# Performance work log

Measured on AMD Instinct MI355X. Metric: run time of the kernel, lower is better.

Reference implementation:

```python
import jax, jax.numpy as jnp
import numpy as np

H = 2        # attention heads (GENsConv heads=2)
DH = 128     # per-head dim (= hidden_channels; concat=False -> heads averaged)
L = 4        # num message-passing layers actually used (convs[:-1])
NG = 500     # number of graphs in the batch
N = 50000    # total nodes
E = 200000   # total edges
HID = 128    # hidden_channels
RES = 0.1    # initial_res
EPS = 1e-5   # BatchNorm eps (eval mode: running_mean=0, running_var=1)


def _bn(x, g, b):
    # BatchNorm1d in eval mode with default running stats
    return x * (g / jnp.sqrt(1.0 + EPS)) + b


def setup_inputs() -> dict:
    key = jax.random.key(0)
    ks = jax.random.split(key, 32)
    s = 0.05
    d = {}
    d["x"] = jax.random.randint(ks[0], (N,), 0, 30)
    d["edge_index"] = jax.random.randint(ks[1], (2, E), 0, N)
    d["edge_attr"] = jax.random.randint(ks[2], (E,), 0, 30)
    d["batch"] = jnp.sort(jax.random.randint(ks[3], (N,), 0, NG))
    d["node_emb"] = jax.random.normal(ks[4], (30, HID)) * s
    d["emb_w1"] = jax.random.normal(ks[5], (HID, HID)) * s
    d["emb_b1"] = jnp.zeros((HID,))
    d["emb_g1"] = jnp.ones((HID,))
    d["emb_bt1"] = jnp.zeros((HID,))
    d["emb_w2"] = jax.random.normal(ks[6], (HID, HID)) * s
    d["emb_b2"] = jnp.zeros((HID,))
    d["bn0_g"] = jnp.ones((HID,))
    d["bn0_b"] = jnp.zeros((HID,))
    d["Wq"] = jax.random.normal(ks[7], (L, HID, H * DH)) * s
    d["Wk"] = jax.random.normal(ks[8], (L, HID, H * DH)) * s
    d["Wv"] = jax.random.normal(ks[9], (L, HID, H * DH)) * s
    d["We"] = jax.random.normal(ks[10], (L, HID, H * DH)) * s
    d["att"] = jax.random.normal(ks[11], (L, H, DH)) * s
    d["Wroot"] = jax.random.normal(ks[12], (L, HID, HID)) * s
    d["bias"] = jnp.zeros((L, HID))
    d["out_w1"] = jax.random.normal(ks[13], (HID * (L + 1), HID)) * s
    d["out_b1"] = jnp.zeros((HID,))
    d["out_g1"] = jnp.ones((HID,))
    d["out_bt1"] = jnp.zeros((HID,))
    d["out_w2"] = jax.random.normal(ks[14], (HID, 1)) * s
    d["out_b2"] = jnp.zeros((1,))
    return d


def _forward(params, x, edge_index, edge_attr, batch):
    (node_emb, emb_w1, emb_b1, emb_g1, emb_bt1, emb_w2, emb_b2, bn0_g, bn0_b,
     Wq, Wk, Wv, We, att, Wroot, bias,
     out_w1, out_b1, out_g1, out_bt1, out_w2, out_b2) = params
    src, dst = edge_index[0], edge_index[1]
    h = node_emb[x]                      # [N, HID]
    ea = node_emb[edge_attr]             # [E, HID] (original embeds edge_attr with node_embedding)
    # emb_convs: Linear -> BN -> ReLU -> Linear, then bns[0] + ReLU
    h = jax.nn.relu(_bn(h @ emb_w1 + emb_b1, emb_g1, emb_bt1))
    h = h @ emb_w2 + emb_b2
    h = jax.nn.relu(_bn(h, bn0_g, bn0_b))
    x0 = h
    xs = [h]
    for i in range(L):
        hi = xs[-1]
        # gather -> per-edge multi-head attention message -> scatter (GENsConv stand-in)
        q = (hi @ Wq[i]).reshape(N, H, DH)[dst]          # [E, H, DH]
        k = (hi @ Wk[i]).reshape(N, H, DH)[src]
        v = (hi @ Wv[i]).reshape(N, H, DH)[src]
        e = (ea @ We[i]).reshape(E, H, DH)
        score = jnp.einsum('ehd,hd->eh', jax.nn.leaky_relu(q + k + e, 0.2), att[i])
        smax = jax.ops.segment_max(score, dst, num_segments=N)[dst]
        exps = jnp.exp(score - smax)
        denom = jax.ops.segment_sum(exps, dst, num_segments=N)[dst]
        alpha = exps / denom                              # segment softmax over incoming edges
        msg = alpha[..., None] * (v + e)                  # [E, H, DH]
        agg = jax.ops.segment_sum(msg, dst, num_segments=N)  # [N, H, DH]
        out = agg.mean(axis=1) + hi @ Wroot[i] + bias[i]  # concat=False -> average heads, + root
        out = jax.nn.relu(out)
        out = (1.0 - RES) * out + RES * x0                # initial residual
        xs.append(out)
    hc = jnp.concatenate(xs, axis=-1)                     # cat=True -> [N, HID*(L+1)]
    sums = jax.ops.segment_sum(hc, batch, num_segments=NG)
    cnt = jax.ops.segment_sum(jnp.ones((N, 1), hc.dtype), batch, num_segments=NG)
    g = sums / jnp.maximum(cnt, 1.0)                      # global mean pool
    g = jax.nn.relu(_bn(g @ out_w1 + out_b1, out_g1, out_bt1))
    g = g @ out_w2 + out_b2
    return g.reshape(-1)                                  # [NG]


def reference(x, edge_index, edge_attr, batch, node_emb, emb_w1, emb_b1, emb_g1, emb_bt1, emb_w2, emb_b2, bn0_g, bn0_b, Wq, Wk, Wv, We, att, Wroot, bias, out_w1, out_b1, out_g1, out_bt1, out_w2, out_b2):
    params = (node_emb, emb_w1, emb_b1, emb_g1, emb_bt1, emb_w2, emb_b2, bn0_g, bn0_b,
              Wq, Wk, Wv, We, att, Wroot, bias,
              out_w1, out_b1, out_g1, out_bt1, out_w2, out_b2)
    return _forward(params, x, edge_index, edge_attr, batch)
```

## Files before the change

### kernel.cpp

```cpp
#include <hip/hip_runtime.h>
#include <hip/hip_bf16.h>

#define NN 50000
#define NE 200000
#define NGR 500
#define HD 128
#define CDIM 256
#define NLAY 4
#define NVOC 30
#define NCAT 896
#define SCH 256
#define SNB ((NN + SCH - 1) / SCH)
#define GP 7
#define CBP (56 / GP)

#define SU_TBLN 30
#define SU_TBLE (NLAY * NVOC)
#define SU_PKW  (NLAY * 224 / 4)
#define SU_HIST ((NE + 255) / 256)
#define SU_NBLK (SU_TBLN + SU_TBLE + SU_PKW + SU_HIST)

static constexpr float BN_INV = 0.9999950000374997f;

typedef __attribute__((ext_vector_type(8))) short bf16x8;
typedef __attribute__((ext_vector_type(4))) float f32x4;
typedef __attribute__((ext_vector_type(2))) float f32x2;

__device__ __forceinline__ float bf2f(unsigned short u) {
    return __uint_as_float(((unsigned)u) << 16);
}
__device__ __forceinline__ unsigned short f2bf(float f) {
    union { __hip_bfloat16 h; unsigned short u; } cv;
    cv.h = __float2bfloat16(f);
    return cv.u;
}
__device__ __forceinline__ f32x2 up2(unsigned u) {
    f32x2 r;
    r.x = __uint_as_float(u << 16);
    r.y = __uint_as_float(u & 0xffff0000u);
    return r;
}
__device__ __forceinline__ f32x2 lk2(f32x2 z) {
    f32x2 zero = {0.f, 0.f};
    return __builtin_elementwise_max(z, zero) + 0.2f * __builtin_elementwise_min(z, zero);
}

__global__ __launch_bounds__(256) void k_setup(
    const float* __restrict__ ne,
    const float* __restrict__ w1, const float* __restrict__ b1,
    const float* __restrict__ g1, const float* __restrict__ bt1,
    const float* __restrict__ w2, const float* __restrict__ b2,
    const float* __restrict__ g0, const float* __restrict__ bt0,
    const float* __restrict__ We,
    const float* __restrict__ Wq, const float* __restrict__ Wk,
    const float* __restrict__ Wv, const float* __restrict__ Wr,
    const int* __restrict__ ei,
    float* __restrict__ x0tab, unsigned short* __restrict__ etab,
    unsigned short* __restrict__ Wpk, int* __restrict__ cnt)
{
    __shared__ float smem[256];
    int b = blockIdx.x, t = threadIdx.x;
    if (b < SU_TBLN) {
        int r = b, d = t;
        if (d < HD) smem[d] = ne[r * HD + d];
        __syncthreads();
        float v1 = 0.f;
        if (d < HD) {
            float acc = b1[d];
            for (int k = 0; k < HD; ++k) acc += smem[k] * w1[k * HD + d];
            v1 = fmaxf(acc * BN_INV * g1[d] + bt1[d], 0.f);
        }
        __syncthreads();
        if (d < HD) smem[HD + d] = v1;
        __syncthreads();
        if (d < HD) {
            float acc2 = b2[d];
            for (int k = 0; k < HD; ++k) acc2 += smem[HD + k] * w2[k * HD + d];
            x0tab[r * HD + d] = fmaxf(acc2 * BN_INV * g0[d] + bt0[d], 0.f);
        }
    } else if (b < SU_TBLN + SU_TBLE) {
        int la = b - SU_TBLN;
        int l = la / NVOC, a = la % NVOC;
        int c = t;
        if (c < HD) smem[c] = ne[a * HD + c];
        __syncthreads();
        const float* W = We + (size_t)l * HD * CDIM;
        float acc = 0.f;
        for (int k = 0; k < HD; ++k) acc += smem[k] * W[k * CDIM + c];
        etab[(size_t)la * CDIM + c] = f2bf(acc);
    } else if (b < SU_TBLN + SU_TBLE + SU_PKW) {
        int bb = (b - SU_TBLN - SU_TBLE) * 4 + (t >> 6);
        int lane = t & 63;
        int l = bb / 224, rem = bb % 224;
        int kb = rem / 56, jb = rem % 56;
        int j = jb * 16 + (lane & 15);
        int kbase = kb * 32 + ((lane >> 4) << 3);
        unsigned short* dst = Wpk + ((size_t)bb * 64 + lane) * 8;
#pragma unroll
        for (int tt = 0; tt < 8; ++tt) {
            int k = kbase + tt;
            float v;
            if (j < 256) {
                v = Wq[((size_t)l * HD + k) * CDIM + j];
            } else if (j < 768) {
                int t2 = j - 256, g = t2 >> 3, r = t2 & 7;
                int c = g * 4 + (r & 3);
                v = (r < 4) ? Wk[((size_t)l * HD + k) * CDIM + c]
                            : Wv[((size_t)l * HD + k) * CDIM + c];
            } else {
                v = Wr[((size_t)l * HD + k) * HD + (j - 768)];
            }
            dst[tt] = f2bf(v);
        }
    } else {
        int e = (b - SU_TBLN - SU_TBLE - SU_PKW) * 256 + t;
        if (e < NE) atomicAdd(&cnt[ei[NE + e]], 1);
    }
}

__global__ __launch_bounds__(256) void k_blocksum(const int* __restrict__ cnt, int* __restrict__ part)
{
    int t = threadIdx.x;
    int i = blockIdx.x * SCH + t;
    int v = (i < NN) ? cnt[i] : 0;
    __shared__ int sm[256];
    sm[t] = v;
    __syncthreads();
    for (int off = 128; off; off >>= 1) {
        if (t < off) sm[t] += sm[t + off];
        __syncthreads();
    }
    if (t == 0) part[blockIdx.x] = sm[0];
}

__global__ __launch_bounds__(256) void k_scanpart(int* __restrict__ part)
{
    int t = threadIdx.x;
    int v = (t < SNB) ? part[t] : 0;
    __shared__ int sm[256];
    sm[t] = v;
    __syncthreads();
    for (int off = 1; off < 256; off <<= 1) {
        int u = (t >= off) ? sm[t - off] : 0;
        __syncthreads();
        sm[t] += u;
        __syncthreads();
    }
    if (t < SNB) part[t] = sm[t] - v;
}

__global__ __launch_bounds__(256) void k_csrwrite(
    const int* __restrict__ cnt, const int* __restrict__ part,
    int* __restrict__ rowp, int* __restrict__ wof)
{
    int t = threadIdx.x;
    int i = blockIdx.x * SCH + t;
    int v = (i < NN) ? cnt[i] : 0;
    __shared__ int sm[256];
    sm[t] = v;
    __syncthreads();
    for (int off = 1; off < 256; off <<= 1) {
        int u = (t >= off) ? sm[t - off] : 0;
        __syncthreads();
        sm[t] += u;
        __syncthreads();
    }
    int excl = sm[t] - v + part[blockIdx.x];
    if (i < NN) { rowp[i] = excl; wof[i] = excl; }
    if (i == NN - 1) rowp[NN] = excl + v;
}

__global__ void k_scatter(const int* __restrict__ ei, const int* __restrict__ ea,
                          int* __restrict__ wof, int2* __restrict__ cse)
{
    int e = blockIdx.x * blockDim.x + threadIdx.x;
    if (e < NE) {
        int d = ei[NE + e];
        int pos = atomicAdd(&wof[d], 1);
        int2 v; v.x = ei[e]; v.y = ea[e];
        cse[pos] = v;
    }
}

__global__ void k_x0(const int* __restrict__ x, const float* __restrict__ tab,
                     unsigned short* __restrict__ x0b,
                     const int* __restrict__ batch, int* __restrict__ gptr)
{
    int idx = blockIdx.x * blockDim.x + threadIdx.x;
    if (idx <= NGR) {
        if (idx == NGR) gptr[idx] = NN;
        else {
            int lo = 0, hi = NN;
            while (lo < hi) { int mid = (lo + hi) >> 1; if (batch[mid] < idx) lo = mid + 1; else hi = mid; }
            gptr[idx] = lo;
        }
    }
    if (idx >= NN * 32) return;
    int n = idx >> 5, c = idx & 31;
    float4 v = *(const float4*)&tab[x[n] * HD + c * 4];
    ushort4 u; u.x = f2bf(v.x); u.y = f2bf(v.y); u.z = f2bf(v.z); u.w = f2bf(v.w);
    *(ushort4*)&x0b[(size_t)n * HD + c * 4] = u;
}

__global__ __launch_bounds__(256) void k_gemm(
    const unsigned short* __restrict__ Ab, const unsigned short* __restrict__ Wpk,
    unsigned short* __restrict__ C)
{
    __shared__ unsigned short tile[64][136];
    int lane = threadIdx.x & 63, wid = threadIdx.x >> 6;
    int nb = blockIdx.x * 64;
    int rowl = wid * 16 + (lane & 15);
    int node = nb + rowl;
    size_t arow = (size_t)((node < NN) ? node : (NN - 1));
    int ko = (lane >> 4) << 3;
    const unsigned short* ap = Ab + arow * HD + ko;
    bf16x8 a0 = *(const bf16x8*)(ap);
    bf16x8 a1 = *(const bf16x8*)(ap + 32);
    bf16x8 a2 = *(const bf16x8*)(ap + 64);
    bf16x8 a3 = *(const bf16x8*)(ap + 96);

    int cb0 = blockIdx.y * CBP;
    const unsigned short* bp = Wpk + (size_t)cb0 * 512 + (size_t)lane * 8;
    int jreg = (lane >> 4) << 2;
#pragma unroll 4
    for (int i = 0; i < CBP; ++i) {
        bf16x8 w0 = *(const bf16x8*)(bp + i * 512);
        bf16x8 w1 = *(const bf16x8*)(bp + i * 512 + 28672);
        bf16x8 w2 = *(const bf16x8*)(bp + i * 512 + 57344);
        bf16x8 w3 = *(const bf16x8*)(bp + i * 512 + 86016);
        f32x4 acc = {0.f, 0.f, 0.f, 0.f};
        acc = __builtin_amdgcn_mfma_f32_16x16x32_bf16(w0, a0, acc, 0, 0, 0);
        acc = __builtin_amdgcn_mfma_f32_16x16x32_bf16(w1, a1, acc, 0, 0, 0);
        acc = __builtin_amdgcn_mfma_f32_16x16x32_bf16(w2, a2, acc, 0, 0, 0);
        acc = __builtin_amdgcn_mfma_f32_16x16x32_bf16(w3, a3, acc, 0, 0, 0);
        uint2 o;
        o.x = (unsigned)f2bf(acc[0]) | ((unsigned)f2bf(acc[1]) << 16);
        o.y = (unsigned)f2bf(acc[2]) | ((unsigned)f2bf(acc[3]) << 16);
        *(uint2*)&tile[rowl][i * 16 + jreg] = o;
    }
    __syncthreads();
    int r0 = threadIdx.x >> 4;
    int cseg = (threadIdx.x & 15) * 8;
#pragma unroll
    for (int pass = 0; pass < 4; ++pass) {
        int row = pass * 16 + r0;
        int gnode = nb + row;
        if (gnode < NN) {
            uint4 v = *(const uint4*)&tile[row][cseg];
            *(uint4*)&C[(size_t)gnode * NCAT + cb0 * 16 + cseg] = v;
        }
    }
}

__global__ __launch_bounds__(256) void k_edge(
    const unsigned short* __restrict__ QKVR,
    const unsigned short* __restrict__ etab,
    const float* __restrict__ attL, const float* __restrict__ biasL,
    const unsigned short* __restrict__ x0b,
    const int* __restrict__ rowptr, const int2* __restrict__ cse,
    unsigned short* __restrict__ hb)
{
    int n = (blockIdx.x * blockDim.x + threadIdx.x) >> 6;
    if (n >= NN) return;
    int lane = threadIdx.x & 63;
    int head = lane >> 5, sub = lane & 31;
    int col = head * HD + sub * 4;
    int kvo = 256 + head * 256 + sub * 8;

    uint2 quu = *(const uint2*)&QKVR[(size_t)n * NCAT + col];
    f32x2 q0 = up2(quu.x), q1 = up2(quu.y);
    float4 a4 = *(const float4*)&attL[col];
    f32x2 av0 = {a4.x, a4.y}, av1 = {a4.z, a4.w};

    float l0 = 0.f, l1 = 0.f;
    f32x2 accA0 = {0.f, 0.f}, accA1 = {0.f, 0.f};
    f32x2 accB0 = {0.f, 0.f}, accB1 = {0.f, 0.f};

    int beg = rowptr[n], end = rowptr[n + 1];
    int idx = beg;
    for (; idx + 1 < end; idx += 2) {
        int2 seA = cse[idx];
        int2 seB = cse[idx + 1];
        uint4 kvA = *(const uint4*)&QKVR[(size_t)seA.x * NCAT + kvo];
        uint4 kvB = *(const uint4*)&QKVR[(size_t)seB.x * NCAT + kvo];
        uint2 euA = *(const uint2*)&etab[seA.y * CDIM + col];
        uint2 euB = *(const uint2*)&etab[seB.y * CDIM + col];

        f32x2 eA0 = up2(euA.x), eA1 = up2(euA.y);
        f32x2 eB0 = up2(euB.x), eB1 = up2(euB.y);

        f32x2 zA0 = lk2(q0 + up2(kvA.x) + eA0);
        f32x2 zA1 = lk2(q1 + up2(kvA.y) + eA1);
        f32x2 zB0 = lk2(q0 + up2(kvB.x) + eB0);
        f32x2 zB1 = lk2(q1 + up2(kvB.y) + eB1);

        f32x2 ppA = zA0 * av0 + zA1 * av1;
        f32x2 ppB = zB0 * av0 + zB1 * av1;
        float pA = ppA.x + ppA.y;
        float pB = ppB.x + ppB.y;
        pA += __shfl_xor(pA, 16); pB += __shfl_xor(pB, 16);
        pA += __shfl_xor(pA, 8);  pB += __shfl_xor(pB, 8);
        pA += __shfl_xor(pA, 4);  pB += __shfl_xor(pB, 4);
        pA += __shfl_xor(pA, 2);  pB += __shfl_xor(pB, 2);
        pA += __shfl_xor(pA, 1);  pB += __shfl_xor(pB, 1);
        float peA = __expf(fminf(fmaxf(pA, -30.f), 30.f));
        float peB = __expf(fminf(fmaxf(pB, -30.f), 30.f));

        accA0 += peA * (up2(kvA.z) + eA0);
        accA1 += peA * (up2(kvA.w) + eA1);
        accB0 += peB * (up2(kvB.z) + eB0);
        accB1 += peB * (up2(kvB.w) + eB1);
        l0 += peA;
        l1 += peB;
    }
    if (idx < end) {
        int2 se = cse[idx];
        uint4 kv = *(const uint4*)&QKVR[(size_t)se.x * NCAT + kvo];
        uint2 eu = *(const uint2*)&etab[se.y * CDIM + col];
        f32x2 e0 = up2(eu.x), e1 = up2(eu.y);
        f32x2 z0 = lk2(q0 + up2(kv.x) + e0);
        f32x2 z1 = lk2(q1 + up2(kv.y) + e1);
        f32x2 pp = z0 * av0 + z1 * av1;
        float p = pp.x + pp.y;
        p += __shfl_xor(p, 16); p += __shfl_xor(p, 8);
        p += __shfl_xor(p, 4);  p += __shfl_xor(p, 2); p += __shfl_xor(p, 1);
        float pe = __expf(fminf(fmaxf(p, -30.f), 30.f));
        accA0 += pe * (up2(kv.z) + e0);
        accA1 += pe * (up2(kv.w) + e1);
        l0 += pe;
    }
    float l = l0 + l1;
    float invl = (l > 0.f) ? 1.0f / l : 0.f;
    f32x2 r0 = (accA0 + accB0) * invl;
    f32x2 r1 = (accA1 + accB1) * invl;
    r0.x = 0.5f * (r0.x + __shfl_xor(r0.x, 32));
    r0.y = 0.5f * (r0.y + __shfl_xor(r0.y, 32));
    r1.x = 0.5f * (r1.x + __shfl_xor(r1.x, 32));
    r1.y = 0.5f * (r1.y + __shfl_xor(r1.y, 32));
    if (head == 0) {
        uint2 ruu = *(const uint2*)&QKVR[(size_t)n * NCAT + 768 + sub * 4];
        f32x2 ru0 = up2(ruu.x), ru1 = up2(ruu.y);
        float4 b4 = *(const float4*)&biasL[sub * 4];
        f32x2 bb0 = {b4.x, b4.y}, bb1 = {b4.z, b4.w};
        uint2 xuu = *(const uint2*)&x0b[(size_t)n * HD + sub * 4];
        f32x2 xx0 = up2(xuu.x), xx1 = up2(xuu.y);
        f32x2 zero = {0.f, 0.f};
        f32x2 h0 = 0.9f * __builtin_elementwise_max(r0 + ru0 + bb0, zero) + 0.1f * xx0;
        f32x2 h1 = 0.9f * __builtin_elementwise_max(r1 + ru1 + bb1, zero) + 0.1f * xx1;
        ushort4 o;
        o.x = f2bf(h0.x); o.y = f2bf(h0.y); o.z = f2bf(h1.x); o.w = f2bf(h1.y);
        *(ushort4*)&hb[(size_t)n * HD + sub * 4] = o;
    }
}

__global__ __launch_bounds__(256) void k_poolall(
    const unsigned short* __restrict__ x0b,
    const unsigned short* __restrict__ h0, const unsigned short* __restrict__ h1,
    const unsigned short* __restrict__ h2, const unsigned short* __restrict__ h3,
    const int* __restrict__ gptr, float* __restrict__ gsum)
{
    int g = blockIdx.x, sl = blockIdx.y;
    const unsigned short* src = (sl == 0) ? x0b : (sl == 1) ? h0 : (sl == 2) ? h1
                              : (sl == 3) ? h2 : h3;
    int q = threadIdx.x & 31;
    int r = threadIdx.x >> 5;
    int beg = gptr[g], end = gptr[g + 1];
    float sx = 0.f, sy = 0.f, sz = 0.f, sw = 0.f;
    for (int n = beg + r; n < end; n += 8) {
        uint2 u = *(const uint2*)&src[(size_t)n * HD + q * 4];
        sx += __uint_as_float(u.x << 16);
        sy += __uint_as_float(u.x & 0xffff0000u);
        sz += __uint_as_float(u.y << 16);
        sw += __uint_as_float(u.y & 0xffff0000u);
    }
    __shared__ float4 sm[8][32];
    float4 s4 = {sx, sy, sz, sw};
    sm[r][q] = s4;
    __syncthreads();
    if (r == 0) {
        float4 t = sm[0][q];
#pragma unroll
        for (int j = 1; j < 8; ++j) {
            float4 u = sm[j][q];
            t.x += u.x; t.y += u.y; t.z += u.z; t.w += u.w;
        }
        *(float4*)&gsum[(size_t)g * 640 + sl * HD + q * 4] = t;
    }
}

__global__ __launch_bounds__(128) void k_out(
    const float* __restrict__ gsum, const int* __restrict__ gptr,
    const float* __restrict__ w1, const float* __restrict__ b1,
    const float* __restrict__ g1, const float* __restrict__ bt1,
    const float* __restrict__ w2, const float* __restrict__ b2,
    float* __restrict__ out)
{
    int g = blockIdx.x, d = threadIdx.x;
    __shared__ float row[640];
    __shared__ float red[2];
    int c = gptr[g + 1] - gptr[g];
    float invc = 1.0f / (float)max(c, 1);
    for (int j = d; j < 640; j += 128) row[j] = gsum[(size_t)g * 640 + j] * invc;
    __syncthreads();
    float acc = b1[d];
    for (int j = 0; j < 640; ++j) acc += row[j] * w1[j * HD + d];
    float val = fmaxf(acc * BN_INV * g1[d] + bt1[d], 0.f);
    float part = val * w2[d];
    part += __shfl_xor(part, 32); part += __shfl_xor(part, 16);
    part += __shfl_xor(part, 8);  part += __shfl_xor(part, 4);
    part += __shfl_xor(part, 2);  part += __shfl_xor(part, 1);
    if ((threadIdx.x & 63) == 0) red[threadIdx.x >> 6] = part;
    __syncthreads();
    if (threadIdx.x == 0) out[g] = red[0] + red[1] + b2[0];
}

extern "C" void kernel_launch(void* const* d_in, const int* in_sizes, int n_in,
                              void* d_out, int out_size, void* d_ws, size_t ws_size,
                              hipStream_t stream)
{
    const int*   x        = (const int*)d_in[0];
    const int*   ei       = (const int*)d_in[1];
    const int*   ea       = (const int*)d_in[2];
    const int*   batch    = (const int*)d_in[3];
    const float* node_emb = (const float*)d_in[4];
    const float* emb_w1   = (const float*)d_in[5];
    const float* emb_b1   = (const float*)d_in[6];
    const float* emb_g1   = (const float*)d_in[7];
    const float* emb_bt1  = (const float*)d_in[8];
    const float* emb_w2   = (const float*)d_in[9];
    const float* emb_b2   = (const float*)d_in[10];
    const float* bn0_g    = (const float*)d_in[11];
    const float* bn0_b    = (const float*)d_in[12];
    const float* Wq       = (const float*)d_in[13];
    const float* Wk       = (const float*)d_in[14];
    const float* Wv       = (const float*)d_in[15];
    const float* We       = (const float*)d_in[16];
    const float* att      = (const float*)d_in[17];
    const float* Wroot    = (const float*)d_in[18];
    const float* bias     = (const float*)d_in[19];
    const float* out_w1   = (const float*)d_in[20];
    const float* out_b1   = (const float*)d_in[21];
    const float* out_g1   = (const float*)d_in[22];
    const float* out_bt1  = (const float*)d_in[23];
    const float* out_w2   = (const float*)d_in[24];
    const float* out_b2   = (const float*)d_in[25];

    char* wp = (char*)d_ws;
    auto alloc = [&](size_t bytes) -> void* {
        void* p = (void*)wp;
        wp += (bytes + 255) & ~(size_t)255;
        return p;
    };
    unsigned short* x0b   = (unsigned short*)alloc((size_t)NN * HD * 2);
    unsigned short* hb0   = (unsigned short*)alloc((size_t)NN * HD * 2);
    unsigned short* hb1   = (unsigned short*)alloc((size_t)NN * HD * 2);
    unsigned short* hb2   = (unsigned short*)alloc((size_t)NN * HD * 2);
    unsigned short* hb3   = (unsigned short*)alloc((size_t)NN * HD * 2);
    unsigned short* QKVR  = (unsigned short*)alloc((size_t)NN * NCAT * 2);
    float*          x0tab = (float*)alloc((size_t)NVOC * HD * 4);
    unsigned short* etab  = (unsigned short*)alloc((size_t)NLAY * NVOC * CDIM * 2);
    unsigned short* Wpk   = (unsigned short*)alloc((size_t)NLAY * 224 * 64 * 8 * 2);
    int*   cnt   = (int*)alloc((size_t)NN * 4);
    int*   rowp  = (int*)alloc((size_t)(NN + 1) * 4);
    int*   wof   = (int*)alloc((size_t)(NN + 1) * 4);
    int*   part  = (int*)alloc((size_t)SNB * 4);
    int2*  cse   = (int2*)alloc((size_t)NE * 8);
    int*   gptr  = (int*)alloc((size_t)(NGR + 1) * 4);
    float* gsum  = (float*)alloc((size_t)NGR * 640 * 4);

    hipMemsetAsync(cnt, 0, (size_t)NN * 4, stream);

    k_setup<<<SU_NBLK, 256, 0, stream>>>(
        node_emb, emb_w1, emb_b1, emb_g1, emb_bt1, emb_w2, emb_b2, bn0_g, bn0_b,
        We, Wq, Wk, Wv, Wroot, ei, x0tab, etab, Wpk, cnt);
    k_blocksum<<<SNB, 256, 0, stream>>>(cnt, part);
    k_scanpart<<<1, 256, 0, stream>>>(part);
    k_csrwrite<<<SNB, 256, 0, stream>>>(cnt, part, rowp, wof);
    k_scatter<<<(NE + 255) / 256, 256, 0, stream>>>(ei, ea, wof, cse);
    k_x0<<<(NN * 32 + 255) / 256, 256, 0, stream>>>(x, x0tab, x0b, batch, gptr);

    const unsigned short* hin = x0b;
    unsigned short* houts[NLAY] = {hb0, hb1, hb2, hb3};
    for (int l = 0; l < NLAY; ++l) {
        k_gemm<<<dim3((NN + 63) / 64, GP), 256, 0, stream>>>(
            hin, Wpk + (size_t)l * 224 * 512, QKVR);
        k_edge<<<(NN * 64 + 255) / 256, 256, 0, stream>>>(
            QKVR, etab + (size_t)l * NVOC * CDIM, att + (size_t)l * CDIM, bias + (size_t)l * HD,
            x0b, rowp, cse, houts[l]);
        hin = houts[l];
    }
    k_poolall<<<dim3(NGR, 5), 256, 0, stream>>>(x0b, hb0, hb1, hb2, hb3, gptr, gsum);
    k_out<<<NGR, 128, 0, stream>>>(gsum, gptr, out_w1, out_b1, out_g1, out_bt1,
                                   out_w2, out_b2, (float*)d_out);
}
```

Baseline: 397.2 us.

## Sort nodes by in-degree bucket so edge-kernel wavefronts get balanced work

Adds a per-node in-degree histogram, a scan and a scatter that build an ordering of nodes grouped by degree. The edge aggregation kernel then maps each wavefront to order[wv] rather than to consecutive nodes, so waves in the same block handle nodes of similar degree and divergent loop lengths are reduced. The cost is three small extra kernels plus an extra indirection. It also loses memory locality for per-node QKVR and output accesses, since consecutive waves now touch scattered node rows.

Result: slower. 619.0 us (+55.8%).

```diff
diff --git a/kernel.cpp b/kernel.cpp
--- a/kernel.cpp
+++ b/kernel.cpp
@@ -13,6 +13,7 @@
 #define SNB ((NN + SCH - 1) / SCH)
 #define GP 7
 #define CBP (56 / GP)
+#define NB 64
 
 #define SU_TBLN 30
 #define SU_TBLE (NLAY * NVOC)
@@ -151,12 +152,14 @@
 
 __global__ __launch_bounds__(256) void k_csrwrite(
     const int* __restrict__ cnt, const int* __restrict__ part,
-    int* __restrict__ rowp, int* __restrict__ wof)
-{
+    int* __restrict__ rowp, int* __restrict__ wof, int* __restrict__ dbin)
+{
+    __shared__ int sm[256];
+    __shared__ int bins[NB];
     int t = threadIdx.x;
+    if (t < NB) bins[t] = 0;
     int i = blockIdx.x * SCH + t;
     int v = (i < NN) ? cnt[i] : 0;
-    __shared__ int sm[256];
     sm[t] = v;
     __syncthreads();
     for (int off = 1; off < 256; off <<= 1) {
@@ -166,8 +169,40 @@
         __syncthreads();
     }
     int excl = sm[t] - v + part[blockIdx.x];
-    if (i < NN) { rowp[i] = excl; wof[i] = excl; }
+    if (i < NN) {
+        rowp[i] = excl; wof[i] = excl;
+        atomicAdd(&bins[min(v, NB - 1)], 1);
+    }
     if (i == NN - 1) rowp[NN] = excl + v;
+    __syncthreads();
+    if (t < NB && bins[t] > 0) atomicAdd(&dbin[t], bins[t]);
+}
+
+__global__ __launch_bounds__(64) void k_dscan(const int* __restrict__ dbin, int* __restrict__ dboff)
+{
+    __shared__ int sm[NB];
+    int t = threadIdx.x;
+    int v = dbin[t];
+    sm[t] = v;
+    __syncthreads();
+    for (int off = 1; off < NB; off <<= 1) {
+        int u = (t >= off) ? sm[t - off] : 0;
+        __syncthreads();
+        sm[t] += u;
+        __syncthreads();
+    }
+    dboff[t] = sm[t] - v;
+}
+
+__global__ void k_dscatter(const int* __restrict__ cnt, int* __restrict__ dboff,
+                           int* __restrict__ order)
+{
+    int n = blockIdx.x * blockDim.x + threadIdx.x;
+    if (n < NN) {
+        int d = min(cnt[n], NB - 1);
+        int pos = atomicAdd(&dboff[d], 1);
+        order[pos] = n;
+    }
 }
 
 __global__ void k_scatter(const int* __restrict__ ei, const int* __restrict__ ea,
@@ -258,10 +293,12 @@
     const float* __restrict__ attL, const float* __restrict__ biasL,
     const unsigned short* __restrict__ x0b,
     const int* __restrict__ rowptr, const int2* __restrict__ cse,
+    const int* __restrict__ order,
     unsigned short* __restrict__ hb)
 {
-    int n = (blockIdx.x * blockDim.x + threadIdx.x) >> 6;
-    if (n >= NN) return;
+    int wv = (blockIdx.x * blockDim.x + threadIdx.x) >> 6;
+    if (wv >= NN) return;
+    int n = order[wv];
     int lane = threadIdx.x & 63;
     int head = lane >> 5, sub = lane & 31;
     int col = head * HD + sub * 4;
@@ -464,18 +501,24 @@
     int*   rowp  = (int*)alloc((size_t)(NN + 1) * 4);
     int*   wof   = (int*)alloc((size_t)(NN + 1) * 4);
     int*   part  = (int*)alloc((size_t)SNB * 4);
+    int*   dbin  = (int*)alloc((size_t)NB * 4);
+    int*   dboff = (int*)alloc((size_t)NB * 4);
+    int*   order = (int*)alloc((size_t)NN * 4);
     int2*  cse   = (int2*)alloc((size_t)NE * 8);
     int*   gptr  = (int*)alloc((size_t)(NGR + 1) * 4);
     float* gsum  = (float*)alloc((size_t)NGR * 640 * 4);
 
     hipMemsetAsync(cnt, 0, (size_t)NN * 4, stream);
+    hipMemsetAsync(dbin, 0, (size_t)NB * 4, stream);
 
     k_setup<<<SU_NBLK, 256, 0, stream>>>(
         node_emb, emb_w1, emb_b1, emb_g1, emb_bt1, emb_w2, emb_b2, bn0_g, bn0_b,
         We, Wq, Wk, Wv, Wroot, ei, x0tab, etab, Wpk, cnt);
     k_blocksum<<<SNB, 256, 0, stream>>>(cnt, part);
     k_scanpart<<<1, 256, 0, stream>>>(part);
-    k_csrwrite<<<SNB, 256, 0, stream>>>(cnt, part, rowp, wof);
+    k_csrwrite<<<SNB, 256, 0, stream>>>(cnt, part, rowp, wof, dbin);
+    k_dscan<<<1, NB, 0, stream>>>(dbin, dboff);
+    k_dscatter<<<SNB, 256, 0, stream>>>(cnt, dboff, order);
     k_scatter<<<(NE + 255) / 256, 256, 0, stream>>>(ei, ea, wof, cse);
     k_x0<<<(NN * 32 + 255) / 256, 256, 0, stream>>>(x, x0tab, x0b, batch, gptr);
 
@@ -486,7 +529,7 @@
             hin, Wpk + (size_t)l * 224 * 512, QKVR);
         k_edge<<<(NN * 64 + 255) / 256, 256, 0, stream>>>(
             QKVR, etab + (size_t)l * NVOC * CDIM, att + (size_t)l * CDIM, bias + (size_t)l * HD,
-            x0b, rowp, cse, houts[l]);
+            x0b, rowp, cse, order, houts[l]);
         hin = houts[l];
     }
     k_poolall<<<dim3(NGR, 5), 256, 0, stream>>>(x0b, hb0, hb1, hb2, hb3, gptr, gsum);
```
